# Kernel optimization log

Hardware: AMD Instinct MI355X
Metric: run time of the kernel (lower is better)

Reference implementation:

```python
import jax, jax.numpy as jnp
import numpy as np

B, GH, GW = 64, 14, 14
H = 512   # features_len == lstm hidden size == lstm_len
E = 512   # embedding_len
A = 512   # attention_len
V = 10000 # wordmap_len
MAXCAP = 50


def setup_inputs() -> dict:
    key = jax.random.key(0)
    ks = jax.random.split(key, 12)
    s = 0.02
    caplens = jax.random.randint(ks[2], (B, 1), 2, MAXCAP + 1, jnp.int32)
    caplens = caplens.at[0, 0].set(MAXCAP)  # ensure max(decode_lengths) == MAXCAP-1 (static T)
    return dict(
        image_features=jax.random.normal(ks[0], (B, GH, GW, H), jnp.float32),
        caps=jax.random.randint(ks[1], (B, MAXCAP), 0, V, jnp.int32),
        caplens=caplens,
        emb_table=jax.random.normal(ks[3], (V, E), jnp.float32) * s,
        W_ih=jax.random.normal(ks[4], (4 * H, E + H), jnp.float32) * s,
        W_hh=jax.random.normal(ks[5], (4 * H, H), jnp.float32) * s,
        b_ih=jnp.zeros((4 * H,), jnp.float32),
        b_hh=jnp.zeros((4 * H,), jnp.float32),
        W_enc=jax.random.normal(ks[6], (A, H), jnp.float32) * s,
        b_enc=jnp.zeros((A,), jnp.float32),
        W_dec=jax.random.normal(ks[7], (A, H), jnp.float32) * s,
        b_dec=jnp.zeros((A,), jnp.float32),
        W_full=jax.random.normal(ks[8], (1, A), jnp.float32) * s,
        b_full=jnp.zeros((1,), jnp.float32),
        W_score=jax.random.normal(ks[9], (V, H), jnp.float32) * s,
        b_score=jnp.zeros((V,), jnp.float32),
    )


def _forward(image_features, emb_table, W_ih, W_hh, b_ih, b_hh,
             W_enc, b_enc, W_dec, b_dec, W_full, b_full, W_score, b_score,
             caps, caplens):
    Bsz = image_features.shape[0]
    feats = image_features.reshape(Bsz, -1, image_features.shape[-1])  # (B, P, H)
    cl = caplens[:, 0]
    sort_ind = jnp.argsort(-cl)                      # descending sort by caption length
    cl = cl[sort_ind]
    feats = feats[sort_ind]
    caps_s = caps[sort_ind]
    decode_lengths = cl - 1
    T = caps.shape[1] - 1                            # static; setup guarantees max(decode_lengths)==T
    emb = emb_table[caps_s]                          # (B, MAXCAP, E)
    enc_att = jnp.einsum('bph,ah->bpa', feats, W_enc) + b_enc  # precomputed encoder attention proj
    mask = jnp.arange(T)[None, :] < decode_lengths[:, None]    # (B, T): row active at step t

    h0 = jnp.zeros((Bsz, feats.shape[-1]), feats.dtype)
    c0 = jnp.zeros_like(h0)

    def step(carry, xs):
        h, c = carry
        emb_t, m_t = xs                              # (B,E), (B,)
        # attention (show-attend-tell style)
        att2 = h @ W_dec.T + b_dec                   # (B, A)
        e = jnp.einsum('bpa,a->bp', jax.nn.relu(enc_att + att2[:, None, :]), W_full[0]) + b_full[0]
        alpha = jax.nn.softmax(e, axis=-1)           # (B, P)
        ctx = jnp.einsum('bp,bph->bh', alpha, feats) # (B, H)
        # LSTMCell
        x = jnp.concatenate([emb_t, ctx], axis=1)    # (B, E+H)
        gates = x @ W_ih.T + b_ih + h @ W_hh.T + b_hh
        i, f, g, o = jnp.split(gates, 4, axis=1)
        c_new = jax.nn.sigmoid(f) * c + jax.nn.sigmoid(i) * jnp.tanh(g)
        h_new = jax.nn.sigmoid(o) * jnp.tanh(c_new)
        score = h_new @ W_score.T + b_score          # (B, V)
        m = m_t[:, None]
        # rows past their decode length keep stale state and write zeros (matches :k slicing)
        h = jnp.where(m, h_new, h)
        c = jnp.where(m, c_new, c)
        return (h, c), (jnp.where(m, score, jnp.zeros((), score.dtype)),
                        jnp.where(m, alpha, jnp.zeros((), alpha.dtype)))

    (_, _), (scores, weights) = jax.lax.scan(
        step, (h0, c0), (emb[:, :T, :].transpose(1, 0, 2), mask.T))
    scores = scores.transpose(1, 0, 2)   # (B, T, V)
    weights = weights.transpose(1, 0, 2) # (B, T, P)
    return scores, caps_s, decode_lengths, weights, sort_ind


def reference(image_features, caps, caplens, emb_table, W_ih, W_hh, b_ih, b_hh,
              W_enc, b_enc, W_dec, b_dec, W_full, b_full, W_score, b_score):
    return _forward(image_features, emb_table, W_ih, W_hh, b_ih, b_hh,
                    W_enc, b_enc, W_dec, b_dec, W_full, b_full, W_score, b_score,
                    caps, caplens)
```

## Files before the change

### kernel.cpp

```cpp
#include <hip/hip_runtime.h>
#include <math.h>


#define WS_SORT   0
#define WS_DL     64
#define WS_NB     128
#define WS_ROWOFF 192
#define WS_CAPS   256
#define WS_RMAP   3456
#define WS_H      6592
#define WS_C      39360
#define WS_ATT2   72128
#define WS_E      104896
#define WS_Z      117696
#define WS_CTXP   117952
#define WS_PG     249024
#define WS_HALL   2346176
#define WS_ENC    3951808

#define OUT_SCORES 0
#define OUT_CAPS   31360000
#define OUT_DL     31363200
#define OUT_W      31363264
#define OUT_SORT   31977920

#define KC  32
#define LST 68

__device__ __forceinline__ float sigm(float x) { return 1.f / (1.f + expf(-x)); }

__device__ __forceinline__ void gemm_acc(const float* __restrict__ As, const float* __restrict__ Bs,
                                         float acc[8][8], int tx, int ty) {
#pragma unroll 8
  for (int kk = 0; kk < KC; ++kk) {
    const float4* ar = (const float4*)(As + kk * LST + tx * 8);
    const float4* br = (const float4*)(Bs + kk * LST + ty * 8);
    float4 a0 = ar[0], a1 = ar[1];
    float4 b0 = br[0], b1 = br[1];
    float av[8] = {a0.x, a0.y, a0.z, a0.w, a1.x, a1.y, a1.z, a1.w};
    float bv[8] = {b0.x, b0.y, b0.z, b0.w, b1.x, b1.y, b1.z, b1.w};
#pragma unroll
    for (int i = 0; i < 8; ++i)
#pragma unroll
      for (int j = 0; j < 8; ++j)
        acc[i][j] = fmaf(av[i], bv[j], acc[i][j]);
  }
}

__device__ __forceinline__ void load_tile_strided(const float* __restrict__ src, int row0, int ld, int k0,
                                                  float* __restrict__ dst, int tid, int nrows_valid) {
#pragma unroll
  for (int i = 0; i < 8; ++i) {
    int lin = tid + 64 * i;
    int m = lin >> 3, kf = lin & 7;
    float4 v = make_float4(0.f, 0.f, 0.f, 0.f);
    if (m < nrows_valid) v = *(const float4*)(src + (long)(row0 + m) * ld + k0 + kf * 4);
    dst[(kf * 4 + 0) * LST + m] = v.x;
    dst[(kf * 4 + 1) * LST + m] = v.y;
    dst[(kf * 4 + 2) * LST + m] = v.z;
    dst[(kf * 4 + 3) * LST + m] = v.w;
  }
}

__device__ __forceinline__ void load_tile_gather(const float* __restrict__ src, const int* __restrict__ bases,
                                                 int k0, float* __restrict__ dst, int tid) {
#pragma unroll
  for (int i = 0; i < 8; ++i) {
    int lin = tid + 64 * i;
    int m = lin >> 3, kf = lin & 7;
    float4 v = *(const float4*)(src + bases[m] + k0 + kf * 4);
    dst[(kf * 4 + 0) * LST + m] = v.x;
    dst[(kf * 4 + 1) * LST + m] = v.y;
    dst[(kf * 4 + 2) * LST + m] = v.z;
    dst[(kf * 4 + 3) * LST + m] = v.w;
  }
}

__global__ __launch_bounds__(64) void setup_kernel(const int* __restrict__ caps, const int* __restrict__ caplens,
                                                   float* __restrict__ ws, float* __restrict__ out) {
  __shared__ int cl_s[64], so_s[64], dl_s[64], nb_s[49], ro_s[50];
  int i = threadIdx.x;
  cl_s[i] = caplens[i];
  __syncthreads();
  int cli = cl_s[i];
  int r = 0;
  for (int j = 0; j < 64; ++j) {
    int clj = cl_s[j];
    r += (clj > cli) || (clj == cli && j < i);
  }
  so_s[r] = i;
  dl_s[r] = cli - 1;
  __syncthreads();
  int* iws = (int*)ws;
  iws[WS_SORT + i] = so_s[i];
  iws[WS_DL + i] = dl_s[i];
  out[OUT_SORT + i] = (float)so_s[i];
  out[OUT_DL + i] = (float)dl_s[i];
  if (i < 49) {
    int n = 0;
    for (int b = 0; b < 64; ++b) n += (dl_s[b] > i);
    iws[WS_NB + i] = n;
    nb_s[i] = n;
  }
  __syncthreads();
  if (i == 0) {
    int acc = 0;
    for (int t = 0; t < 49; ++t) { ro_s[t] = acc; acc += nb_s[t]; }
    ro_s[49] = acc;
    iws[WS_NB + 49] = acc;
  }
  __syncthreads();
  if (i < 50) iws[WS_ROWOFF + i] = ro_s[i];
  int R = ro_s[49];
  for (int rr = i; rr < 3136; rr += 64) {
    int val = 0;
    if (rr < R) {
      int t = 0;
      while (t < 48 && ro_s[t + 1] <= rr) ++t;
      val = t * 64 + (rr - ro_s[t]);
    }
    iws[WS_RMAP + rr] = val;
  }
  for (int j = i; j < 3200; j += 64) {
    int k = j / 50, jj = j - k * 50;
    int cv = caps[so_s[k] * 50 + jj];
    iws[WS_CAPS + j] = cv;
    out[OUT_CAPS + j] = (float)cv;
  }
}

__global__ void zero_init_kernel(float* __restrict__ out, float* __restrict__ ws, const float* __restrict__ b_dec) {
  const float4 z = make_float4(0.f, 0.f, 0.f, 0.f);
  float4* out4 = (float4*)out;
  float4* ws4 = (float4*)ws;
  const float4* bd4 = (const float4*)b_dec;
  for (long idx = (long)blockIdx.x * 256 + threadIdx.x; idx < 8018240L; idx += (long)gridDim.x * 256) {
    if (idx < 7840000L) {
      out4[idx] = z;
    } else if (idx < 7993664L) {
      out4[7840816L + (idx - 7840000L)] = z;
    } else if (idx < 8010048L) {
      ws4[1648L + (idx - 7993664L)] = z;
    } else {
      long j = idx - 8010048L;
      ws4[18032L + j] = bd4[j & 127];
    }
  }
}

__global__ __launch_bounds__(64) void encatt_kernel(const float* __restrict__ image, const float* __restrict__ W_enc,
                                                    const float* __restrict__ b_enc, float* __restrict__ ws) {
  __shared__ __align__(16) float As[KC * LST];
  __shared__ __align__(16) float Bs[KC * LST];
  __shared__ int rb[64];
  int tid = threadIdx.x;
  const int* iws = (const int*)ws;
  int mt = blockIdx.x, nt = blockIdx.y;
  {
    int r = mt * 64 + tid;
    int b = r / 196;
    int p = r - b * 196;
    rb[tid] = iws[WS_SORT + b] * 100352 + p * 512;
  }
  float acc[8][8] = {};
  for (int ch = 0; ch < 16; ++ch) {
    __syncthreads();
    load_tile_gather(image, rb, ch * 32, As, tid);
    load_tile_strided(W_enc, nt * 64, 512, ch * 32, Bs, tid, 64);
    __syncthreads();
    gemm_acc(As, Bs, acc, tid & 7, tid >> 3);
  }
  int tx = tid & 7, ty = tid >> 3;
  int r0 = mt * 64 + tx * 8;
  int n0 = nt * 64 + ty * 8;
#pragma unroll
  for (int i = 0; i < 8; ++i) {
    float* cp = ws + WS_ENC + (long)(r0 + i) * 512 + n0;
    *(float4*)(cp)     = make_float4(acc[i][0] + b_enc[n0],     acc[i][1] + b_enc[n0 + 1],
                                     acc[i][2] + b_enc[n0 + 2], acc[i][3] + b_enc[n0 + 3]);
    *(float4*)(cp + 4) = make_float4(acc[i][4] + b_enc[n0 + 4], acc[i][5] + b_enc[n0 + 5],
                                     acc[i][6] + b_enc[n0 + 6], acc[i][7] + b_enc[n0 + 7]);
  }
}

__global__ __launch_bounds__(256) void ectx_kernel(float* __restrict__ ws, const float* __restrict__ image,
                                                   const float* __restrict__ W_full, const float* __restrict__ b_full,
                                                   int t) {
  const int* iws = (const int*)ws;
  int b = blockIdx.x;
  if (b >= iws[WS_NB + t]) return;
  int pg = blockIdx.y;
  __shared__ float att2_s[512], wf_s[512], e_s[52];
  int tid = threadIdx.x;
  for (int a = tid; a < 512; a += 256) {
    att2_s[a] = ws[WS_ATT2 + b * 512 + a];
    wf_s[a] = W_full[a];
  }
  __syncthreads();
  int w = tid >> 6, lane = tid & 63;
  float bf0 = b_full[0];
  for (int idx = w; idx < 49; idx += 4) {
    int p = pg * 49 + idx;
    const float* er = ws + WS_ENC + (long)(b * 196 + p) * 512;
    float acc = 0.f;
#pragma unroll
    for (int a8 = 0; a8 < 8; ++a8) {
      int a = (a8 << 6) + lane;
      float v = er[a] + att2_s[a];
      acc = fmaf(fmaxf(v, 0.f), wf_s[a], acc);
    }
#pragma unroll
    for (int off = 32; off; off >>= 1) acc += __shfl_down(acc, off);
    if (lane == 0) e_s[idx] = expf(acc + bf0);
  }
  __syncthreads();
  if (tid < 49) ws[WS_E + b * 200 + pg * 49 + tid] = e_s[tid];
  if (tid == 0) {
    float zz = 0.f;
    for (int j = 0; j < 49; ++j) zz += e_s[j];
    ws[WS_Z + pg * 64 + b] = zz;
  }
  long sb = (long)iws[WS_SORT + b] * 100352;
  float a0 = 0.f, a1 = 0.f;
  for (int j = 0; j < 49; ++j) {
    float al = e_s[j];
    const float* fp = image + sb + (long)(pg * 49 + j) * 512;
    a0 = fmaf(al, fp[tid], a0);
    a1 = fmaf(al, fp[tid + 256], a1);
  }
  ws[WS_CTXP + pg * 32768 + b * 512 + tid] = a0;
  ws[WS_CTXP + pg * 32768 + b * 512 + 256 + tid] = a1;
}

__global__ __launch_bounds__(64) void gates_kernel(float* __restrict__ ws, const float* __restrict__ emb,
                                                   const float* __restrict__ W_ih, const float* __restrict__ W_hh,
                                                   int t) {
  __shared__ __align__(16) float As[KC * LST];
  __shared__ __align__(16) float Bs[KC * LST];
  __shared__ int rbe[64];
  __shared__ float rcpz_s[64];
  int tid = threadIdx.x;
  int nt = blockIdx.x;
  int ks = blockIdx.y;
  int* iws = (int*)ws;
  rbe[tid] = iws[WS_CAPS + tid * 50 + t] * 512;
  {
    float zz = ws[WS_Z + tid] + ws[WS_Z + 64 + tid] + ws[WS_Z + 128 + tid] + ws[WS_Z + 192 + tid];
    rcpz_s[tid] = 1.f / zz;
  }
  float acc[8][8] = {};
  for (int ch = 0; ch < 3; ++ch) {
    int k0 = ks * 96 + ch * 32;
    __syncthreads();
    if (k0 < 512) {
      load_tile_gather(emb, rbe, k0, As, tid);
    } else if (k0 < 1024) {
      int kc = k0 - 512;
#pragma unroll
      for (int i = 0; i < 8; ++i) {
        int lin = tid + 64 * i;
        int m = lin >> 3, kf = lin & 7;
        const float* base = ws + WS_CTXP + m * 512 + kc + kf * 4;
        float4 v0 = *(const float4*)(base);
        float4 v1 = *(const float4*)(base + 32768);
        float4 v2 = *(const float4*)(base + 65536);
        float4 v3 = *(const float4*)(base + 98304);
        float rz = rcpz_s[m];
        As[(kf * 4 + 0) * LST + m] = (v0.x + v1.x + v2.x + v3.x) * rz;
        As[(kf * 4 + 1) * LST + m] = (v0.y + v1.y + v2.y + v3.y) * rz;
        As[(kf * 4 + 2) * LST + m] = (v0.z + v1.z + v2.z + v3.z) * rz;
        As[(kf * 4 + 3) * LST + m] = (v0.w + v1.w + v2.w + v3.w) * rz;
      }
    } else {
      load_tile_strided(ws + WS_H, 0, 512, k0 - 1024, As, tid, 64);
    }
    if (k0 < 1024) load_tile_strided(W_ih, nt * 64, 1024, k0, Bs, tid, 64);
    else           load_tile_strided(W_hh, nt * 64, 512, k0 - 1024, Bs, tid, 64);
    __syncthreads();
    gemm_acc(As, Bs, acc, tid & 7, tid >> 3);
  }
  int tx = tid & 7, ty = tid >> 3;
  float* pg = ws + WS_PG + ks * 131072;
  int j0 = nt * 64 + ty * 8;
#pragma unroll
  for (int i = 0; i < 8; ++i) {
    int b = tx * 8 + i;
    float* cp = pg + b * 2048 + j0;
    *(float4*)(cp)     = make_float4(acc[i][0], acc[i][1], acc[i][2], acc[i][3]);
    *(float4*)(cp + 4) = make_float4(acc[i][4], acc[i][5], acc[i][6], acc[i][7]);
  }
}

__global__ __launch_bounds__(512) void lstm_att2_kernel(float* __restrict__ ws, const float* __restrict__ b_ih,
                                                        const float* __restrict__ b_hh, const float* __restrict__ W_dec,
                                                        const float* __restrict__ b_dec, float* __restrict__ out, int t) {
  const int* iws = (const int*)ws;
  int b = blockIdx.x;
  int as = blockIdx.y;
  int hh = threadIdx.x;
  int nb = iws[WS_NB + t];
  __shared__ float h_s[512], red[512];
  float gi = b_ih[hh] + b_hh[hh];
  float gf = b_ih[512 + hh] + b_hh[512 + hh];
  float gg = b_ih[1024 + hh] + b_hh[1024 + hh];
  float go = b_ih[1536 + hh] + b_hh[1536 + hh];
  const float* pgp = ws + WS_PG + b * 2048;
#pragma unroll
  for (int ks = 0; ks < 16; ++ks) {
    const float* p = pgp + ks * 131072;
    gi += p[hh]; gf += p[512 + hh]; gg += p[1024 + hh]; go += p[1536 + hh];
  }
  float c = ws[WS_C + b * 512 + hh];
  float cn = sigm(gf) * c + sigm(gi) * tanhf(gg);
  float hn = sigm(go) * tanhf(cn);
  h_s[hh] = hn;
  if (b < nb) {
    if (as == 0) {
      ws[WS_C + b * 512 + hh] = cn;
      ws[WS_H + b * 512 + hh] = hn;
      ws[WS_HALL + (long)(iws[WS_ROWOFF + t] + b) * 512 + hh] = hn;
    }
    if (hh < 49) {
      float zz = ws[WS_Z + b] + ws[WS_Z + 64 + b] + ws[WS_Z + 128 + b] + ws[WS_Z + 192 + b];
      int p = as * 49 + hh;
      out[OUT_W + (long)(b * 49 + t) * 196 + p] = ws[WS_E + b * 200 + p] / zz;
    }
  }
  __syncthreads();
  int a = as * 128 + (hh >> 2);
  int part = hh & 3;
  const float* wd = W_dec + (long)a * 512 + part * 128;
  const float* hp = h_s + part * 128;
  float s = 0.f;
#pragma unroll 8
  for (int j = 0; j < 32; ++j) {
    float4 wv = *(const float4*)(wd + 4 * j);
    s = fmaf(hp[4 * j], wv.x, s);
    s = fmaf(hp[4 * j + 1], wv.y, s);
    s = fmaf(hp[4 * j + 2], wv.z, s);
    s = fmaf(hp[4 * j + 3], wv.w, s);
  }
  red[hh] = s;
  __syncthreads();
  if (part == 0) {
    float v = red[hh] + red[hh + 1] + red[hh + 2] + red[hh + 3] + b_dec[a];
    ws[WS_ATT2 + b * 512 + a] = v;
  }
}

__global__ __launch_bounds__(64) void score_kernel(const float* __restrict__ ws, const float* __restrict__ W_score,
                                                   const float* __restrict__ b_score, float* __restrict__ out) {
  __shared__ __align__(16) float As[KC * LST];
  __shared__ __align__(16) float Bs[KC * LST];
  const int* iws = (const int*)ws;
  int mt = blockIdx.x, nt = blockIdx.y;
  int R = iws[WS_NB + 49];
  if (mt * 64 >= R) return;
  int tid = threadIdx.x;
  int mvalid = R - mt * 64; if (mvalid > 64) mvalid = 64;
  int nvalid = 10000 - nt * 64; if (nvalid > 64) nvalid = 64;
  float acc[8][8] = {};
  for (int ch = 0; ch < 16; ++ch) {
    __syncthreads();
    load_tile_strided(ws + WS_HALL, mt * 64, 512, ch * 32, As, tid, mvalid);
    load_tile_strided(W_score, nt * 64, 512, ch * 32, Bs, tid, nvalid);
    __syncthreads();
    gemm_acc(As, Bs, acc, tid & 7, tid >> 3);
  }
  int tx = tid & 7, ty = tid >> 3;
  int n0 = nt * 64 + ty * 8;
#pragma unroll
  for (int i = 0; i < 8; ++i) {
    int r = mt * 64 + tx * 8 + i;
    if (r >= R) continue;
    int tb = iws[WS_RMAP + r];
    int bb = tb & 63, tt = tb >> 6;
    float* cp = out + (long)bb * 490000 + tt * 10000 + n0;
    if (n0 + 4 <= 10000)
      *(float4*)(cp)     = make_float4(acc[i][0] + b_score[n0],     acc[i][1] + b_score[n0 + 1],
                                       acc[i][2] + b_score[n0 + 2], acc[i][3] + b_score[n0 + 3]);
    if (n0 + 8 <= 10000)
      *(float4*)(cp + 4) = make_float4(acc[i][4] + b_score[n0 + 4], acc[i][5] + b_score[n0 + 5],
                                       acc[i][6] + b_score[n0 + 6], acc[i][7] + b_score[n0 + 7]);
  }
}

extern "C" void kernel_launch(void* const* d_in, const int* in_sizes, int n_in,
                              void* d_out, int out_size, void* d_ws, size_t ws_size,
                              hipStream_t stream) {
  const float* image   = (const float*)d_in[0];
  const int*   caps    = (const int*)d_in[1];
  const int*   caplens = (const int*)d_in[2];
  const float* emb     = (const float*)d_in[3];
  const float* W_ih    = (const float*)d_in[4];
  const float* W_hh    = (const float*)d_in[5];
  const float* b_ih    = (const float*)d_in[6];
  const float* b_hh    = (const float*)d_in[7];
  const float* W_enc   = (const float*)d_in[8];
  const float* b_enc   = (const float*)d_in[9];
  const float* W_dec   = (const float*)d_in[10];
  const float* b_dec   = (const float*)d_in[11];
  const float* W_full  = (const float*)d_in[12];
  const float* b_full  = (const float*)d_in[13];
  const float* W_score = (const float*)d_in[14];
  const float* b_score = (const float*)d_in[15];
  float* out = (float*)d_out;
  float* ws  = (float*)d_ws;

  setup_kernel<<<1, 64, 0, stream>>>(caps, caplens, ws, out);
  zero_init_kernel<<<2048, 256, 0, stream>>>(out, ws, b_dec);
  encatt_kernel<<<dim3(196, 8), 64, 0, stream>>>(image, W_enc, b_enc, ws);
  for (int t = 0; t < 49; ++t) {
    ectx_kernel<<<dim3(64, 4), 256, 0, stream>>>(ws, image, W_full, b_full, t);
    gates_kernel<<<dim3(32, 16), 64, 0, stream>>>(ws, emb, W_ih, W_hh, t);
    lstm_att2_kernel<<<dim3(64, 4), 512, 0, stream>>>(ws, b_ih, b_hh, W_dec, b_dec, out, t);
  }
  score_kernel<<<dim3(49, 157), 64, 0, stream>>>(ws, W_score, b_score, out);
}
```

Before: 2.873 ms.

## Enlarge GEMM tiles to 128x128 with 256-thread blocks and widen per-step kernels

The encoder-attention and score GEMMs move from 64x64 tiles with 64 threads to 128x128 tiles with 256 threads, using a swizzled shared-memory layout and a K-chunk of 16. The gates kernel now stages its whole 96-wide K slice in one pass with 256 threads that each compute an 8x2 output, and ectx uses 512 threads so each thread handles one context column. The goal is more threads per block, better latency hiding and more data reuse per shared-memory load. The cost is more shared memory and registers per block and fewer blocks in the grid.

```diff
diff --git a/kernel.cpp b/kernel.cpp
--- a/kernel.cpp
+++ b/kernel.cpp
@@ -24,17 +24,53 @@
 #define OUT_W      31363264
 #define OUT_SORT   31977920
 
-#define KC  32
-#define LST 68
+#define LSW 196
 
 __device__ __forceinline__ float sigm(float x) { return 1.f / (1.f + expf(-x)); }
 
-__device__ __forceinline__ void gemm_acc(const float* __restrict__ As, const float* __restrict__ Bs,
-                                         float acc[8][8], int tx, int ty) {
-#pragma unroll 8
-  for (int kk = 0; kk < KC; ++kk) {
-    const float4* ar = (const float4*)(As + kk * LST + tx * 8);
-    const float4* br = (const float4*)(Bs + kk * LST + ty * 8);
+__device__ __forceinline__ float4 f4add(float4 a, float4 b) {
+  return make_float4(a.x + b.x, a.y + b.y, a.z + b.z, a.w + b.w);
+}
+
+__device__ __forceinline__ int swz128(int m) { return (m >> 3) * 12 + (m & 7); }
+
+__device__ __forceinline__ void stage128_strided(const float* __restrict__ src, int row0, int ld, int k0,
+                                                 float* __restrict__ dst, int tid, int nrows_valid) {
+#pragma unroll
+  for (int i = 0; i < 2; ++i) {
+    int lin = tid + 256 * i;
+    int m = lin >> 2, kf = lin & 3;
+    float4 v = make_float4(0.f, 0.f, 0.f, 0.f);
+    if (m < nrows_valid) v = *(const float4*)(src + (long)(row0 + m) * ld + k0 + kf * 4);
+    int mc = swz128(m);
+    dst[(kf * 4 + 0) * LSW + mc] = v.x;
+    dst[(kf * 4 + 1) * LSW + mc] = v.y;
+    dst[(kf * 4 + 2) * LSW + mc] = v.z;
+    dst[(kf * 4 + 3) * LSW + mc] = v.w;
+  }
+}
+
+__device__ __forceinline__ void stage128_gather(const float* __restrict__ src, const int* __restrict__ bases,
+                                                int k0, float* __restrict__ dst, int tid) {
+#pragma unroll
+  for (int i = 0; i < 2; ++i) {
+    int lin = tid + 256 * i;
+    int m = lin >> 2, kf = lin & 3;
+    float4 v = *(const float4*)(src + bases[m] + k0 + kf * 4);
+    int mc = swz128(m);
+    dst[(kf * 4 + 0) * LSW + mc] = v.x;
+    dst[(kf * 4 + 1) * LSW + mc] = v.y;
+    dst[(kf * 4 + 2) * LSW + mc] = v.z;
+    dst[(kf * 4 + 3) * LSW + mc] = v.w;
+  }
+}
+
+__device__ __forceinline__ void gemm_acc128(const float* __restrict__ As, const float* __restrict__ Bs,
+                                            float acc[8][8], int tx, int ty) {
+#pragma unroll
+  for (int kk = 0; kk < 16; ++kk) {
+    const float4* ar = (const float4*)(As + kk * LSW + tx * 12);
+    const float4* br = (const float4*)(Bs + kk * LSW + ty * 12);
     float4 a0 = ar[0], a1 = ar[1];
     float4 b0 = br[0], b1 = br[1];
     float av[8] = {a0.x, a0.y, a0.z, a0.w, a1.x, a1.y, a1.z, a1.w};
@@ -44,35 +80,6 @@
 #pragma unroll
       for (int j = 0; j < 8; ++j)
         acc[i][j] = fmaf(av[i], bv[j], acc[i][j]);
-  }
-}
-
-__device__ __forceinline__ void load_tile_strided(const float* __restrict__ src, int row0, int ld, int k0,
-                                                  float* __restrict__ dst, int tid, int nrows_valid) {
-#pragma unroll
-  for (int i = 0; i < 8; ++i) {
-    int lin = tid + 64 * i;
-    int m = lin >> 3, kf = lin & 7;
-    float4 v = make_float4(0.f, 0.f, 0.f, 0.f);
-    if (m < nrows_valid) v = *(const float4*)(src + (long)(row0 + m) * ld + k0 + kf * 4);
-    dst[(kf * 4 + 0) * LST + m] = v.x;
-    dst[(kf * 4 + 1) * LST + m] = v.y;
-    dst[(kf * 4 + 2) * LST + m] = v.z;
-    dst[(kf * 4 + 3) * LST + m] = v.w;
-  }
-}
-
-__device__ __forceinline__ void load_tile_gather(const float* __restrict__ src, const int* __restrict__ bases,
-                                                 int k0, float* __restrict__ dst, int tid) {
-#pragma unroll
-  for (int i = 0; i < 8; ++i) {
-    int lin = tid + 64 * i;
-    int m = lin >> 3, kf = lin & 7;
-    float4 v = *(const float4*)(src + bases[m] + k0 + kf * 4);
-    dst[(kf * 4 + 0) * LST + m] = v.x;
-    dst[(kf * 4 + 1) * LST + m] = v.y;
-    dst[(kf * 4 + 2) * LST + m] = v.z;
-    dst[(kf * 4 + 3) * LST + m] = v.w;
   }
 }
 
@@ -148,31 +155,31 @@
   }
 }
 
-__global__ __launch_bounds__(64) void encatt_kernel(const float* __restrict__ image, const float* __restrict__ W_enc,
-                                                    const float* __restrict__ b_enc, float* __restrict__ ws) {
-  __shared__ __align__(16) float As[KC * LST];
-  __shared__ __align__(16) float Bs[KC * LST];
-  __shared__ int rb[64];
+__global__ __launch_bounds__(256) void encatt_kernel(const float* __restrict__ image, const float* __restrict__ W_enc,
+                                                     const float* __restrict__ b_enc, float* __restrict__ ws) {
+  __shared__ __align__(16) float As[16 * LSW];
+  __shared__ __align__(16) float Bs[16 * LSW];
+  __shared__ int rb[128];
   int tid = threadIdx.x;
   const int* iws = (const int*)ws;
   int mt = blockIdx.x, nt = blockIdx.y;
-  {
-    int r = mt * 64 + tid;
+  if (tid < 128) {
+    int r = mt * 128 + tid;
     int b = r / 196;
     int p = r - b * 196;
     rb[tid] = iws[WS_SORT + b] * 100352 + p * 512;
   }
   float acc[8][8] = {};
-  for (int ch = 0; ch < 16; ++ch) {
+  for (int ch = 0; ch < 32; ++ch) {
     __syncthreads();
-    load_tile_gather(image, rb, ch * 32, As, tid);
-    load_tile_strided(W_enc, nt * 64, 512, ch * 32, Bs, tid, 64);
+    stage128_gather(image, rb, ch * 16, As, tid);
+    stage128_strided(W_enc, nt * 128, 512, ch * 16, Bs, tid, 128);
     __syncthreads();
-    gemm_acc(As, Bs, acc, tid & 7, tid >> 3);
-  }
-  int tx = tid & 7, ty = tid >> 3;
-  int r0 = mt * 64 + tx * 8;
-  int n0 = nt * 64 + ty * 8;
+    gemm_acc128(As, Bs, acc, tid & 15, tid >> 4);
+  }
+  int tx = tid & 15, ty = tid >> 4;
+  int r0 = mt * 128 + tx * 8;
+  int n0 = nt * 128 + ty * 8;
 #pragma unroll
   for (int i = 0; i < 8; ++i) {
     float* cp = ws + WS_ENC + (long)(r0 + i) * 512 + n0;
@@ -183,7 +190,7 @@
   }
 }
 
-__global__ __launch_bounds__(256) void ectx_kernel(float* __restrict__ ws, const float* __restrict__ image,
+__global__ __launch_bounds__(512) void ectx_kernel(float* __restrict__ ws, const float* __restrict__ image,
                                                    const float* __restrict__ W_full, const float* __restrict__ b_full,
                                                    int t) {
   const int* iws = (const int*)ws;
@@ -192,14 +199,12 @@
   int pg = blockIdx.y;
   __shared__ float att2_s[512], wf_s[512], e_s[52];
   int tid = threadIdx.x;
-  for (int a = tid; a < 512; a += 256) {
-    att2_s[a] = ws[WS_ATT2 + b * 512 + a];
-    wf_s[a] = W_full[a];
-  }
+  att2_s[tid] = ws[WS_ATT2 + b * 512 + tid];
+  wf_s[tid] = W_full[tid];
   __syncthreads();
   int w = tid >> 6, lane = tid & 63;
   float bf0 = b_full[0];
-  for (int idx = w; idx < 49; idx += 4) {
+  for (int idx = w; idx < 49; idx += 8) {
     int p = pg * 49 + idx;
     const float* er = ws + WS_ENC + (long)(b * 196 + p) * 512;
     float acc = 0.f;
@@ -221,73 +226,84 @@
     ws[WS_Z + pg * 64 + b] = zz;
   }
   long sb = (long)iws[WS_SORT + b] * 100352;
-  float a0 = 0.f, a1 = 0.f;
+  float a0 = 0.f;
   for (int j = 0; j < 49; ++j) {
-    float al = e_s[j];
-    const float* fp = image + sb + (long)(pg * 49 + j) * 512;
-    a0 = fmaf(al, fp[tid], a0);
-    a1 = fmaf(al, fp[tid + 256], a1);
+    a0 = fmaf(e_s[j], image[sb + (long)(pg * 49 + j) * 512 + tid], a0);
   }
   ws[WS_CTXP + pg * 32768 + b * 512 + tid] = a0;
-  ws[WS_CTXP + pg * 32768 + b * 512 + 256 + tid] = a1;
-}
-
-__global__ __launch_bounds__(64) void gates_kernel(float* __restrict__ ws, const float* __restrict__ emb,
-                                                   const float* __restrict__ W_ih, const float* __restrict__ W_hh,
-                                                   int t) {
-  __shared__ __align__(16) float As[KC * LST];
-  __shared__ __align__(16) float Bs[KC * LST];
+}
+
+__global__ __launch_bounds__(256) void gates_kernel(float* __restrict__ ws, const float* __restrict__ emb,
+                                                    const float* __restrict__ W_ih, const float* __restrict__ W_hh,
+                                                    int t) {
+  __shared__ __align__(16) float As[96 * 68];
+  __shared__ __align__(16) float Bs[96 * 68];
   __shared__ int rbe[64];
   __shared__ float rcpz_s[64];
   int tid = threadIdx.x;
   int nt = blockIdx.x;
   int ks = blockIdx.y;
   int* iws = (int*)ws;
-  rbe[tid] = iws[WS_CAPS + tid * 50 + t] * 512;
-  {
+  if (tid < 64) {
+    rbe[tid] = iws[WS_CAPS + tid * 50 + t] * 512;
     float zz = ws[WS_Z + tid] + ws[WS_Z + 64 + tid] + ws[WS_Z + 128 + tid] + ws[WS_Z + 192 + tid];
     rcpz_s[tid] = 1.f / zz;
   }
-  float acc[8][8] = {};
-  for (int ch = 0; ch < 3; ++ch) {
-    int k0 = ks * 96 + ch * 32;
-    __syncthreads();
-    if (k0 < 512) {
-      load_tile_gather(emb, rbe, k0, As, tid);
-    } else if (k0 < 1024) {
-      int kc = k0 - 512;
-#pragma unroll
-      for (int i = 0; i < 8; ++i) {
-        int lin = tid + 64 * i;
-        int m = lin >> 3, kf = lin & 7;
-        const float* base = ws + WS_CTXP + m * 512 + kc + kf * 4;
+  __syncthreads();
+#pragma unroll
+  for (int c = 0; c < 3; ++c) {
+    int k0 = ks * 96 + c * 32;
+#pragma unroll
+    for (int i = 0; i < 2; ++i) {
+      int lin = tid + 256 * i;
+      int kf = lin >> 6;
+      int m = lin & 63;
+      float4 v;
+      if (k0 < 512) {
+        v = *(const float4*)(emb + (long)rbe[m] + k0 + kf * 4);
+      } else if (k0 < 1024) {
+        const float* base = ws + WS_CTXP + m * 512 + (k0 - 512) + kf * 4;
         float4 v0 = *(const float4*)(base);
         float4 v1 = *(const float4*)(base + 32768);
         float4 v2 = *(const float4*)(base + 65536);
         float4 v3 = *(const float4*)(base + 98304);
         float rz = rcpz_s[m];
-        As[(kf * 4 + 0) * LST + m] = (v0.x + v1.x + v2.x + v3.x) * rz;
-        As[(kf * 4 + 1) * LST + m] = (v0.y + v1.y + v2.y + v3.y) * rz;
-        As[(kf * 4 + 2) * LST + m] = (v0.z + v1.z + v2.z + v3.z) * rz;
-        As[(kf * 4 + 3) * LST + m] = (v0.w + v1.w + v2.w + v3.w) * rz;
+        v = make_float4((v0.x + v1.x + v2.x + v3.x) * rz, (v0.y + v1.y + v2.y + v3.y) * rz,
+                        (v0.z + v1.z + v2.z + v3.z) * rz, (v0.w + v1.w + v2.w + v3.w) * rz);
+      } else {
+        v = *(const float4*)(ws + WS_H + m * 512 + (k0 - 1024) + kf * 4);
       }
-    } else {
-      load_tile_strided(ws + WS_H, 0, 512, k0 - 1024, As, tid, 64);
-    }
-    if (k0 < 1024) load_tile_strided(W_ih, nt * 64, 1024, k0, Bs, tid, 64);
-    else           load_tile_strided(W_hh, nt * 64, 512, k0 - 1024, Bs, tid, 64);
-    __syncthreads();
-    gemm_acc(As, Bs, acc, tid & 7, tid >> 3);
-  }
-  int tx = tid & 7, ty = tid >> 3;
+      float* da = As + (c * 32 + kf * 4) * 68 + m;
+      da[0] = v.x; da[68] = v.y; da[136] = v.z; da[204] = v.w;
+      const float* srcB = (k0 < 1024) ? (W_ih + (long)(nt * 64 + m) * 1024 + k0 + kf * 4)
+                                      : (W_hh + (long)(nt * 64 + m) * 512 + (k0 - 1024) + kf * 4);
+      float4 bv = *(const float4*)srcB;
+      float* db = Bs + (c * 32 + kf * 4) * 68 + m;
+      db[0] = bv.x; db[68] = bv.y; db[136] = bv.z; db[204] = bv.w;
+    }
+  }
+  __syncthreads();
+  int w = tid >> 6, lane = tid & 63;
+  int tx = lane & 7, ty = lane >> 3;
+  float acc[8][2] = {};
+#pragma unroll 8
+  for (int kk = 0; kk < 96; ++kk) {
+    const float4* ar = (const float4*)(As + kk * 68 + tx * 8);
+    float4 a0 = ar[0], a1 = ar[1];
+    float2 bv = *(const float2*)(Bs + kk * 68 + w * 16 + ty * 2);
+    float av[8] = {a0.x, a0.y, a0.z, a0.w, a1.x, a1.y, a1.z, a1.w};
+#pragma unroll
+    for (int i = 0; i < 8; ++i) {
+      acc[i][0] = fmaf(av[i], bv.x, acc[i][0]);
+      acc[i][1] = fmaf(av[i], bv.y, acc[i][1]);
+    }
+  }
   float* pg = ws + WS_PG + ks * 131072;
-  int j0 = nt * 64 + ty * 8;
+  int j0 = nt * 64 + w * 16 + ty * 2;
 #pragma unroll
   for (int i = 0; i < 8; ++i) {
     int b = tx * 8 + i;
-    float* cp = pg + b * 2048 + j0;
-    *(float4*)(cp)     = make_float4(acc[i][0], acc[i][1], acc[i][2], acc[i][3]);
-    *(float4*)(cp + 4) = make_float4(acc[i][4], acc[i][5], acc[i][6], acc[i][7]);
+    *(float2*)(pg + b * 2048 + j0) = make_float2(acc[i][0], acc[i][1]);
   }
 }
 
@@ -348,30 +364,30 @@
   }
 }
 
-__global__ __launch_bounds__(64) void score_kernel(const float* __restrict__ ws, const float* __restrict__ W_score,
-                                                   const float* __restrict__ b_score, float* __restrict__ out) {
-  __shared__ __align__(16) float As[KC * LST];
-  __shared__ __align__(16) float Bs[KC * LST];
+__global__ __launch_bounds__(256) void score_kernel(const float* __restrict__ ws, const float* __restrict__ W_score,
+                                                    const float* __restrict__ b_score, float* __restrict__ out) {
+  __shared__ __align__(16) float As[16 * LSW];
+  __shared__ __align__(16) float Bs[16 * LSW];
   const int* iws = (const int*)ws;
   int mt = blockIdx.x, nt = blockIdx.y;
   int R = iws[WS_NB + 49];
-  if (mt * 64 >= R) return;
+  if (mt * 128 >= R) return;
   int tid = threadIdx.x;
-  int mvalid = R - mt * 64; if (mvalid > 64) mvalid = 64;
-  int nvalid = 10000 - nt * 64; if (nvalid > 64) nvalid = 64;
+  int mvalid = R - mt * 128; if (mvalid > 128) mvalid = 128;
+  int nvalid = 10000 - nt * 128; if (nvalid > 128) nvalid = 128;
   float acc[8][8] = {};
-  for (int ch = 0; ch < 16; ++ch) {
+  for (int ch = 0; ch < 32; ++ch) {
     __syncthreads();
-    load_tile_strided(ws + WS_HALL, mt * 64, 512, ch * 32, As, tid, mvalid);
-    load_tile_strided(W_score, nt * 64, 512, ch * 32, Bs, tid, nvalid);
+    stage128_strided(ws + WS_HALL, mt * 128, 512, ch * 16, As, tid, mvalid);
+    stage128_strided(W_score, nt * 128, 512, ch * 16, Bs, tid, nvalid);
     __syncthreads();
-    gemm_acc(As, Bs, acc, tid & 7, tid >> 3);
-  }
-  int tx = tid & 7, ty = tid >> 3;
-  int n0 = nt * 64 + ty * 8;
+    gemm_acc128(As, Bs, acc, tid & 15, tid >> 4);
+  }
+  int tx = tid & 15, ty = tid >> 4;
+  int n0 = nt * 128 + ty * 8;
 #pragma unroll
   for (int i = 0; i < 8; ++i) {
-    int r = mt * 64 + tx * 8 + i;
+    int r = mt * 128 + tx * 8 + i;
     if (r >= R) continue;
     int tb = iws[WS_RMAP + r];
     int bb = tb & 63, tt = tb >> 6;
@@ -409,11 +425,11 @@
 
   setup_kernel<<<1, 64, 0, stream>>>(caps, caplens, ws, out);
   zero_init_kernel<<<2048, 256, 0, stream>>>(out, ws, b_dec);
-  encatt_kernel<<<dim3(196, 8), 64, 0, stream>>>(image, W_enc, b_enc, ws);
+  encatt_kernel<<<dim3(98, 4), 256, 0, stream>>>(image, W_enc, b_enc, ws);
   for (int t = 0; t < 49; ++t) {
-    ectx_kernel<<<dim3(64, 4), 256, 0, stream>>>(ws, image, W_full, b_full, t);
-    gates_kernel<<<dim3(32, 16), 64, 0, stream>>>(ws, emb, W_ih, W_hh, t);
+    ectx_kernel<<<dim3(64, 4), 512, 0, stream>>>(ws, image, W_full, b_full, t);
+    gates_kernel<<<dim3(32, 16), 256, 0, stream>>>(ws, emb, W_ih, W_hh, t);
     lstm_att2_kernel<<<dim3(64, 4), 512, 0, stream>>>(ws, b_ih, b_hh, W_dec, b_dec, out, t);
   }
-  score_kernel<<<dim3(49, 157), 64, 0, stream>>>(ws, W_score, b_score, out);
-}
+  score_kernel<<<dim3(25, 79), 256, 0, stream>>>(ws, W_score, b_score, out);
+}
```

After: 2.378 ms. -17.2%, faster.
